# Kernel tuning notes

Hardware: AMD Instinct MI355X
Metric: run time of the kernel (lower is better)

The kernel has to match this reference:

```python
import jax, jax.numpy as jnp
import numpy as np

N = 100000   # nodes
E = 1600000  # edges
F_IN = 32    # num_features
H = 16       # hidden_size (hardcoded as conv2 input in source)
C = 10       # num_classes
K = 2        # kernel_size (dim=1)


def setup_inputs() -> dict:
    key = jax.random.key(0)
    ks = jax.random.split(key, 9)
    x = jax.random.normal(ks[0], (N, F_IN), dtype=jnp.float32)
    edge_index = jax.random.randint(ks[1], (2, E), 0, N, dtype=jnp.int64)
    edge_attr = jax.random.uniform(ks[2], (E, 1), dtype=jnp.float32)
    s1 = 1.0 / np.sqrt(F_IN)
    s2 = 1.0 / np.sqrt(H)
    W1 = jax.random.normal(ks[3], (K, F_IN, H), dtype=jnp.float32) * s1
    root1 = jax.random.normal(ks[4], (F_IN, H), dtype=jnp.float32) * s1
    b1 = jnp.zeros((H,), dtype=jnp.float32)
    W2 = jax.random.normal(ks[5], (K, H, C), dtype=jnp.float32) * s2
    root2 = jax.random.normal(ks[6], (H, C), dtype=jnp.float32) * s2
    b2 = jnp.zeros((C,), dtype=jnp.float32)
    return {"x": x, "edge_index": edge_index, "edge_attr": edge_attr,
            "W1": W1, "root1": root1, "b1": b1,
            "W2": W2, "root2": root2, "b2": b2}


def spline_conv(x, edge_index, edge_attr, W, root, bias, num_nodes):
    # Open B-spline, degree 1: hat-function basis over K knots.
    k = W.shape[0]
    src, dst = edge_index[0], edge_index[1]
    v = edge_attr[:, 0] * (k - 1)                                   # [E]
    grid = jnp.arange(k, dtype=v.dtype)
    basis = jnp.maximum(0.0, 1.0 - jnp.abs(v[:, None] - grid[None, :]))  # [E,K]
    xe = x[src]                                                      # [E,in] gather
    msg = jnp.einsum('ei,kio,ek->eo', xe, W, basis)                  # per-edge message
    agg = jax.ops.segment_sum(msg, dst, num_segments=num_nodes)      # scatter-add
    deg = jax.ops.segment_sum(jnp.ones((msg.shape[0],), x.dtype), dst,
                              num_segments=num_nodes)
    agg = agg / jnp.maximum(deg, 1.0)[:, None]                       # mean aggregation
    return agg + x @ root + bias


def reference(x, edge_index, edge_attr, W1, root1, b1, W2, root2, b2):
    # Inference mode: F.dropout(training=False) is identity.
    h = jax.nn.elu(spline_conv(x, edge_index, edge_attr, W1, root1, b1, N))
    out = spline_conv(h, edge_index, edge_attr, W2, root2, b2, N)
    return jax.nn.log_softmax(out, axis=1)
```

## Files before the change

kernel.cpp:

```cpp
#include <hip/hip_runtime.h>
#include <math.h>

#define N_NODES 100000
#define E_EDGES 1600000
#define F_IN 32
#define HID 16
#define NC 10
#define SRC_BITS 17
#define SRC_MASK ((1u << SRC_BITS) - 1u)
#define VQ_SCALE 32767.0f
#define CBITS 8
#define BUCKET_N 256
#define NCB ((N_NODES + BUCKET_N - 1) / BUCKET_N)
#define BLK_E 4096
#define NBLK ((E_EDGES + BLK_E - 1) / BLK_E)
#define L1_BLOCKS ((N_NODES + 511) / 512)
#define CAP 6144

__device__ __forceinline__ unsigned int bf16pair(float lo, float hi) {
    unsigned int ulo = __float_as_uint(lo), uhi = __float_as_uint(hi);
    ulo += 0x7fffu + ((ulo >> 16) & 1u);
    uhi += 0x7fffu + ((uhi >> 16) & 1u);
    return (ulo >> 16) | (uhi & 0xffff0000u);
}

__device__ __forceinline__ float lerp_pair(unsigned int pair, float v) {
    float a = __uint_as_float(pair << 16);
    float b = __uint_as_float(pair & 0xffff0000u);
    return fmaf(v, b - a, a);
}

__global__ __launch_bounds__(512) void fused_l1bucket(
    const float* __restrict__ x, const float* __restrict__ W1,
    const float* __restrict__ root1, const float* __restrict__ b1,
    const int* __restrict__ ei, const float* __restrict__ ea,
    unsigned int* __restrict__ y, float* __restrict__ r1,
    int* __restrict__ gcur, int2* __restrict__ ebuf)
{
    if (blockIdx.x >= L1_BLOCKS) {
        __shared__ int h[NCB], base[NCB], cur[NCB];
        int t = threadIdx.x;
        int b = blockIdx.x - L1_BLOCKS;
        for (int i = t; i < NCB; i += 512) { h[i] = 0; cur[i] = 0; }
        __syncthreads();

        const int* dstp = ei + E_EDGES;
        int e0 = b * BLK_E + t * 8;
        int4 dA, dB, sA, sB;
        float4 aA, aB;
        bool fullA = (e0 + 3 < E_EDGES), fullB = (e0 + 7 < E_EDGES);
        if (fullA) {
            dA = *(const int4*)(dstp + e0);
            sA = *(const int4*)(ei + e0);
            aA = *(const float4*)(ea + e0);
            atomicAdd(&h[dA.x >> CBITS], 1);
            atomicAdd(&h[dA.y >> CBITS], 1);
            atomicAdd(&h[dA.z >> CBITS], 1);
            atomicAdd(&h[dA.w >> CBITS], 1);
        }
        if (fullB) {
            dB = *(const int4*)(dstp + e0 + 4);
            sB = *(const int4*)(ei + e0 + 4);
            aB = *(const float4*)(ea + e0 + 4);
            atomicAdd(&h[dB.x >> CBITS], 1);
            atomicAdd(&h[dB.y >> CBITS], 1);
            atomicAdd(&h[dB.z >> CBITS], 1);
            atomicAdd(&h[dB.w >> CBITS], 1);
        }
        if (!fullA || !fullB) {
            int lo = fullA ? e0 + 4 : e0;
            for (int e = lo; e < E_EDGES && e < e0 + 8; e++)
                atomicAdd(&h[dstp[e] >> CBITS], 1);
        }
        __syncthreads();

        for (int s = t; s < NCB; s += 512)
            if (h[s] > 0) base[s] = atomicAdd(&gcur[s], h[s]);
        __syncthreads();

        if (fullA) {
            {
                int s = dA.x >> CBITS;
                int idx = base[s] + atomicAdd(&cur[s], 1);
                unsigned int vq = (unsigned int)(aA.x * VQ_SCALE + 0.5f);
                if (idx < CAP)
                    ebuf[(size_t)s * CAP + idx] = make_int2(dA.x & (BUCKET_N - 1),
                        (int)((vq << SRC_BITS) | (unsigned int)sA.x));
            }
            {
                int s = dA.y >> CBITS;
                int idx = base[s] + atomicAdd(&cur[s], 1);
                unsigned int vq = (unsigned int)(aA.y * VQ_SCALE + 0.5f);
                if (idx < CAP)
                    ebuf[(size_t)s * CAP + idx] = make_int2(dA.y & (BUCKET_N - 1),
                        (int)((vq << SRC_BITS) | (unsigned int)sA.y));
            }
            {
                int s = dA.z >> CBITS;
                int idx = base[s] + atomicAdd(&cur[s], 1);
                unsigned int vq = (unsigned int)(aA.z * VQ_SCALE + 0.5f);
                if (idx < CAP)
                    ebuf[(size_t)s * CAP + idx] = make_int2(dA.z & (BUCKET_N - 1),
                        (int)((vq << SRC_BITS) | (unsigned int)sA.z));
            }
            {
                int s = dA.w >> CBITS;
                int idx = base[s] + atomicAdd(&cur[s], 1);
                unsigned int vq = (unsigned int)(aA.w * VQ_SCALE + 0.5f);
                if (idx < CAP)
                    ebuf[(size_t)s * CAP + idx] = make_int2(dA.w & (BUCKET_N - 1),
                        (int)((vq << SRC_BITS) | (unsigned int)sA.w));
            }
        }
        if (fullB) {
            {
                int s = dB.x >> CBITS;
                int idx = base[s] + atomicAdd(&cur[s], 1);
                unsigned int vq = (unsigned int)(aB.x * VQ_SCALE + 0.5f);
                if (idx < CAP)
                    ebuf[(size_t)s * CAP + idx] = make_int2(dB.x & (BUCKET_N - 1),
                        (int)((vq << SRC_BITS) | (unsigned int)sB.x));
            }
            {
                int s = dB.y >> CBITS;
                int idx = base[s] + atomicAdd(&cur[s], 1);
                unsigned int vq = (unsigned int)(aB.y * VQ_SCALE + 0.5f);
                if (idx < CAP)
                    ebuf[(size_t)s * CAP + idx] = make_int2(dB.y & (BUCKET_N - 1),
                        (int)((vq << SRC_BITS) | (unsigned int)sB.y));
            }
            {
                int s = dB.z >> CBITS;
                int idx = base[s] + atomicAdd(&cur[s], 1);
                unsigned int vq = (unsigned int)(aB.z * VQ_SCALE + 0.5f);
                if (idx < CAP)
                    ebuf[(size_t)s * CAP + idx] = make_int2(dB.z & (BUCKET_N - 1),
                        (int)((vq << SRC_BITS) | (unsigned int)sB.z));
            }
            {
                int s = dB.w >> CBITS;
                int idx = base[s] + atomicAdd(&cur[s], 1);
                unsigned int vq = (unsigned int)(aB.w * VQ_SCALE + 0.5f);
                if (idx < CAP)
                    ebuf[(size_t)s * CAP + idx] = make_int2(dB.w & (BUCKET_N - 1),
                        (int)((vq << SRC_BITS) | (unsigned int)sB.w));
            }
        }
        if (!fullA || !fullB) {
            int lo = fullA ? e0 + 4 : e0;
            for (int e = lo; e < E_EDGES && e < e0 + 8; e++) {
                int dst = dstp[e];
                int s = dst >> CBITS;
                int idx = base[s] + atomicAdd(&cur[s], 1);
                unsigned int vq = (unsigned int)(ea[e] * VQ_SCALE + 0.5f);
                if (idx < CAP)
                    ebuf[(size_t)s * CAP + idx] = make_int2(dst & (BUCKET_N - 1),
                        (int)((vq << SRC_BITS) | (unsigned int)ei[e]));
            }
        }
        return;
    }
    __shared__ float sW0[F_IN * HID], sW1[F_IN * HID], sR[F_IN * HID], sB[HID];
    for (int i = threadIdx.x; i < F_IN * HID; i += 512) {
        sW0[i] = W1[i];
        sW1[i] = W1[F_IN * HID + i];
        sR[i]  = root1[i];
    }
    if (threadIdx.x < HID) sB[threadIdx.x] = b1[threadIdx.x];
    __syncthreads();

    int n = blockIdx.x * 512 + threadIdx.x;
    if (n >= N_NODES) return;

    float xr[F_IN];
    const float4* xp = (const float4*)(x + (size_t)n * F_IN);
    #pragma unroll
    for (int i = 0; i < F_IN / 4; i++) {
        float4 t4 = xp[i];
        xr[i*4+0] = t4.x; xr[i*4+1] = t4.y; xr[i*4+2] = t4.z; xr[i*4+3] = t4.w;
    }

    float a0[HID], a1[HID], ar[HID];
    #pragma unroll
    for (int o = 0; o < HID; o++) { a0[o] = 0.f; a1[o] = 0.f; ar[o] = sB[o]; }
    for (int i = 0; i < F_IN; i++) {
        float xi = xr[i];
        #pragma unroll
        for (int o = 0; o < HID; o++) {
            a0[o] += xi * sW0[i * HID + o];
            a1[o] += xi * sW1[i * HID + o];
            ar[o] += xi * sR[i * HID + o];
        }
    }
    unsigned int* py = y + (size_t)n * 16;
    float* pr = r1 + (size_t)n * HID;
    #pragma unroll
    for (int o = 0; o < HID; o++) {
        py[o] = bf16pair(a0[o], a1[o]);
        pr[o] = ar[o];
    }
}

__global__ __launch_bounds__(1024) void k_bsort(
    const int2* __restrict__ ebuf, const int* __restrict__ gcur,
    unsigned int* __restrict__ es, int* __restrict__ start)
{
    __shared__ int hist[BUCKET_N];
    __shared__ int cursor[BUCKET_N];
    __shared__ int pre[NCB];
    __shared__ int wsum[16], woff[16];
    __shared__ int wsum2[4], woff2[4];
    int t = threadIdx.x;
    int b = blockIdx.x;
    int w = t >> 6, l = t & 63;

    int v = (t < NCB) ? min(gcur[t], CAP) : 0;
    int incl = v;
    #pragma unroll
    for (int off = 1; off < 64; off <<= 1) {
        int u = __shfl_up(incl, off, 64);
        if (l >= off) incl += u;
    }
    if (l == 63) wsum[w] = incl;
    if (t < BUCKET_N) { hist[t] = 0; cursor[t] = 0; }
    __syncthreads();
    if (t == 0) {
        int a = 0;
        #pragma unroll
        for (int i = 0; i < 16; i++) { woff[i] = a; a += wsum[i]; }
    }
    __syncthreads();
    if (t < NCB) pre[t] = woff[w] + incl - v;
    __syncthreads();

    int fill = min(gcur[b], CAP);
    int obase = pre[b];
    const int2* win = ebuf + (size_t)b * CAP;

    for (int j = t; j < fill; j += 1024)
        atomicAdd(&hist[win[j].x], 1);
    __syncthreads();

    int c = (t < BUCKET_N) ? hist[t] : 0;
    int incl2 = c;
    #pragma unroll
    for (int off = 1; off < 64; off <<= 1) {
        int u = __shfl_up(incl2, off, 64);
        if (l >= off) incl2 += u;
    }
    if (w < 4 && l == 63) wsum2[w] = incl2;
    __syncthreads();
    if (t == 0) {
        int acc = 0;
        #pragma unroll
        for (int i = 0; i < 4; i++) { woff2[i] = acc; acc += wsum2[i]; }
    }
    __syncthreads();
    if (t < BUCKET_N) {
        int excl = woff2[w] + incl2 - c;
        hist[t] = excl;
        int node = (b << CBITS) + t;
        if (node < N_NODES) start[node] = obase + excl;
    }
    if (b == 0 && t == 0) start[N_NODES] = E_EDGES;
    __syncthreads();

    for (int j = t; j < fill; j += 1024) {
        int2 p = win[j];
        int off = atomicAdd(&cursor[p.x], 1);
        es[obase + hist[p.x] + off] = (unsigned int)p.y;
    }
}

__global__ __launch_bounds__(256) void k_agg1(
    const unsigned int* __restrict__ es, const int* __restrict__ start,
    const unsigned int* __restrict__ y, const float* __restrict__ r1,
    const float* __restrict__ W2, const float* __restrict__ root2,
    const float* __restrict__ b2,
    unsigned int* __restrict__ z, float* __restrict__ r2)
{
    __shared__ float sW0[HID * NC], sW1[HID * NC], sRt[HID * NC], sB2[NC];
    int t = threadIdx.x;
    if (t < HID * NC) { sW0[t] = W2[t]; sW1[t] = W2[HID * NC + t]; sRt[t] = root2[t]; }
    if (t >= HID * NC && t < HID * NC + NC) sB2[t - HID * NC] = b2[t - HID * NC];
    __syncthreads();

    int idx = blockIdx.x * 256 + t;
    int n = idx >> 2, l = idx & 3;
    if (n >= N_NODES) return;
    int j0 = start[n], j1 = start[n + 1];
    const uint4* yrow = (const uint4*)y;
    float acc[4] = {0.f, 0.f, 0.f, 0.f};
    int j = j0;
    for (; j + 3 < j1; j += 4) {
        unsigned int p0 = es[j], p1 = es[j+1], p2 = es[j+2], p3 = es[j+3];
        uint4 q0 = yrow[(size_t)(p0 & SRC_MASK) * 4 + l];
        uint4 q1 = yrow[(size_t)(p1 & SRC_MASK) * 4 + l];
        uint4 q2 = yrow[(size_t)(p2 & SRC_MASK) * 4 + l];
        uint4 q3 = yrow[(size_t)(p3 & SRC_MASK) * 4 + l];
        float v0 = (float)(p0 >> SRC_BITS) * (1.0f / VQ_SCALE);
        float v1 = (float)(p1 >> SRC_BITS) * (1.0f / VQ_SCALE);
        float v2 = (float)(p2 >> SRC_BITS) * (1.0f / VQ_SCALE);
        float v3 = (float)(p3 >> SRC_BITS) * (1.0f / VQ_SCALE);
        acc[0] += lerp_pair(q0.x, v0); acc[1] += lerp_pair(q0.y, v0);
        acc[2] += lerp_pair(q0.z, v0); acc[3] += lerp_pair(q0.w, v0);
        acc[0] += lerp_pair(q1.x, v1); acc[1] += lerp_pair(q1.y, v1);
        acc[2] += lerp_pair(q1.z, v1); acc[3] += lerp_pair(q1.w, v1);
        acc[0] += lerp_pair(q2.x, v2); acc[1] += lerp_pair(q2.y, v2);
        acc[2] += lerp_pair(q2.z, v2); acc[3] += lerp_pair(q2.w, v2);
        acc[0] += lerp_pair(q3.x, v3); acc[1] += lerp_pair(q3.y, v3);
        acc[2] += lerp_pair(q3.z, v3); acc[3] += lerp_pair(q3.w, v3);
    }
    for (; j < j1; j++) {
        unsigned int p = es[j];
        uint4 q = yrow[(size_t)(p & SRC_MASK) * 4 + l];
        float v = (float)(p >> SRC_BITS) * (1.0f / VQ_SCALE);
        acc[0] += lerp_pair(q.x, v); acc[1] += lerp_pair(q.y, v);
        acc[2] += lerp_pair(q.z, v); acc[3] += lerp_pair(q.w, v);
    }
    float inv = 1.0f / fmaxf((float)(j1 - j0), 1.0f);
    float4 rr = *(const float4*)(r1 + (size_t)n * HID + l * 4);
    float hv[4];
    hv[0] = acc[0] * inv + rr.x;
    hv[1] = acc[1] * inv + rr.y;
    hv[2] = acc[2] * inv + rr.z;
    hv[3] = acc[3] * inv + rr.w;
    #pragma unroll
    for (int e = 0; e < 4; e++) hv[e] = hv[e] > 0.0f ? hv[e] : expm1f(hv[e]);

    int cbase = l * 4;
    float a0[4] = {0.f, 0.f, 0.f, 0.f}, a1[4] = {0.f, 0.f, 0.f, 0.f}, ar[4];
    #pragma unroll
    for (int e = 0; e < 4; e++) { int c = cbase + e; ar[e] = (c < NC) ? sB2[c] : 0.f; }
    #pragma unroll
    for (int s = 0; s < 4; s++) {
        #pragma unroll
        for (int e2 = 0; e2 < 4; e2++) {
            float hi = __shfl(hv[e2], s, 4);
            int i = s * 4 + e2;
            #pragma unroll
            for (int e = 0; e < 4; e++) {
                int c = cbase + e;
                if (c < NC) {
                    a0[e] += hi * sW0[i * NC + c];
                    a1[e] += hi * sW1[i * NC + c];
                    ar[e] += hi * sRt[i * NC + c];
                }
            }
        }
    }
    uint4 zo;
    zo.x = (cbase + 0 < NC) ? bf16pair(a0[0], a1[0]) : 0u;
    zo.y = (cbase + 1 < NC) ? bf16pair(a0[1], a1[1]) : 0u;
    zo.z = (cbase + 2 < NC) ? bf16pair(a0[2], a1[2]) : 0u;
    zo.w = (cbase + 3 < NC) ? bf16pair(a0[3], a1[3]) : 0u;
    ((uint4*)z)[(size_t)n * 4 + l] = zo;
    #pragma unroll
    for (int e = 0; e < 4; e++) {
        int c = cbase + e;
        if (c < NC) r2[(size_t)n * NC + c] = ar[e];
    }
}

__global__ __launch_bounds__(256) void k_agg2(
    const unsigned int* __restrict__ es, const int* __restrict__ start,
    const unsigned int* __restrict__ z,
    const float* __restrict__ r2, float* __restrict__ out)
{
    int idx = blockIdx.x * 256 + threadIdx.x;
    int n = idx >> 2, l = idx & 3;
    if (n >= N_NODES) return;
    int j0 = start[n], j1 = start[n + 1];
    const uint4* zrow = (const uint4*)z;
    float acc[4] = {0.f, 0.f, 0.f, 0.f};
    int j = j0;
    for (; j + 3 < j1; j += 4) {
        unsigned int p0 = es[j], p1 = es[j+1], p2 = es[j+2], p3 = es[j+3];
        uint4 q0 = zrow[(size_t)(p0 & SRC_MASK) * 4 + l];
        uint4 q1 = zrow[(size_t)(p1 & SRC_MASK) * 4 + l];
        uint4 q2 = zrow[(size_t)(p2 & SRC_MASK) * 4 + l];
        uint4 q3 = zrow[(size_t)(p3 & SRC_MASK) * 4 + l];
        float v0 = (float)(p0 >> SRC_BITS) * (1.0f / VQ_SCALE);
        float v1 = (float)(p1 >> SRC_BITS) * (1.0f / VQ_SCALE);
        float v2 = (float)(p2 >> SRC_BITS) * (1.0f / VQ_SCALE);
        float v3 = (float)(p3 >> SRC_BITS) * (1.0f / VQ_SCALE);
        acc[0] += lerp_pair(q0.x, v0); acc[1] += lerp_pair(q0.y, v0);
        acc[2] += lerp_pair(q0.z, v0); acc[3] += lerp_pair(q0.w, v0);
        acc[0] += lerp_pair(q1.x, v1); acc[1] += lerp_pair(q1.y, v1);
        acc[2] += lerp_pair(q1.z, v1); acc[3] += lerp_pair(q1.w, v1);
        acc[0] += lerp_pair(q2.x, v2); acc[1] += lerp_pair(q2.y, v2);
        acc[2] += lerp_pair(q2.z, v2); acc[3] += lerp_pair(q2.w, v2);
        acc[0] += lerp_pair(q3.x, v3); acc[1] += lerp_pair(q3.y, v3);
        acc[2] += lerp_pair(q3.z, v3); acc[3] += lerp_pair(q3.w, v3);
    }
    for (; j < j1; j++) {
        unsigned int p = es[j];
        uint4 q = zrow[(size_t)(p & SRC_MASK) * 4 + l];
        float v = (float)(p >> SRC_BITS) * (1.0f / VQ_SCALE);
        acc[0] += lerp_pair(q.x, v); acc[1] += lerp_pair(q.y, v);
        acc[2] += lerp_pair(q.z, v); acc[3] += lerp_pair(q.w, v);
    }
    float inv = 1.0f / fmaxf((float)(j1 - j0), 1.0f);
    int cbase = l * 4;
    float val[4];
    #pragma unroll
    for (int e = 0; e < 4; e++) {
        int c = cbase + e;
        val[e] = (c < NC) ? acc[e] * inv + r2[(size_t)n * NC + c] : -INFINITY;
    }
    float mx = fmaxf(fmaxf(val[0], val[1]), fmaxf(val[2], val[3]));
    mx = fmaxf(mx, __shfl_xor(mx, 1, 4));
    mx = fmaxf(mx, __shfl_xor(mx, 2, 4));
    float ssum = 0.f;
    #pragma unroll
    for (int e = 0; e < 4; e++) {
        int c = cbase + e;
        if (c < NC) ssum += expf(val[e] - mx);
    }
    ssum += __shfl_xor(ssum, 1, 4);
    ssum += __shfl_xor(ssum, 2, 4);
    float lse = logf(ssum);
    #pragma unroll
    for (int e = 0; e < 4; e++) {
        int c = cbase + e;
        if (c < NC) out[(size_t)n * NC + c] = val[e] - mx - lse;
    }
}

extern "C" void kernel_launch(void* const* d_in, const int* in_sizes, int n_in,
                              void* d_out, int out_size, void* d_ws, size_t ws_size,
                              hipStream_t stream) {
    const float* x     = (const float*)d_in[0];
    const int*   ei    = (const int*)d_in[1];
    const float* ea    = (const float*)d_in[2];
    const float* W1    = (const float*)d_in[3];
    const float* root1 = (const float*)d_in[4];
    const float* b1    = (const float*)d_in[5];
    const float* W2    = (const float*)d_in[6];
    const float* root2 = (const float*)d_in[7];
    const float* b2    = (const float*)d_in[8];
    float* out = (float*)d_out;

    char* wsb = (char*)d_ws;
    int2*         ebuf   = (int2*)wsb;
    unsigned int* es     = (unsigned int*)(wsb + (size_t)NCB * CAP * 8);
    unsigned int* y      = es + (size_t)E_EDGES;
    float*        r1     = (float*)(y + (size_t)N_NODES * 16);
    unsigned int* z      = (unsigned int*)(r1 + (size_t)N_NODES * HID);
    float*        r2     = (float*)(z + (size_t)N_NODES * 16);
    int*          start  = (int*)(r2 + (size_t)N_NODES * NC);
    int*          gcur   = start + N_NODES + 1;

    int aggGrid = (N_NODES * 4 + 255) / 256;

    hipMemsetAsync(gcur, 0, (size_t)NCB * sizeof(int), stream);
    fused_l1bucket<<<L1_BLOCKS + NBLK, 512, 0, stream>>>(x, W1, root1, b1, ei, ea,
                                                         y, r1, gcur, ebuf);
    k_bsort<<<NCB, 1024, 0, stream>>>(ebuf, gcur, es, start);
    k_agg1 <<<aggGrid, 256, 0, stream>>>(es, start, y, r1, W2, root2, b2, z, r2);
    k_agg2 <<<aggGrid, 256, 0, stream>>>(es, start, z, r2, out);
}
```

Before: 176.1 us.

## Split bucket buffer into byte and word arrays, enlarge edge blocks, unroll gathers

Replaces the int2 bucket buffer with a separate byte array for the local destination and a word array for the packed payload. This cuts bucket-stage write and read traffic from 8 to 5 bytes per edge. Doubles the edges handled per scatter block (16 per thread) to amortize the shared histogram setup and the global atomics. Adds 8-way unrolled gather loops to both aggregation kernels for more memory-level parallelism, at the cost of higher register pressure.

```diff
diff --git a/kernel.cpp b/kernel.cpp
--- a/kernel.cpp
+++ b/kernel.cpp
@@ -12,7 +12,7 @@
 #define CBITS 8
 #define BUCKET_N 256
 #define NCB ((N_NODES + BUCKET_N - 1) / BUCKET_N)
-#define BLK_E 4096
+#define BLK_E 8192
 #define NBLK ((E_EDGES + BLK_E - 1) / BLK_E)
 #define L1_BLOCKS ((N_NODES + 511) / 512)
 #define CAP 6144
@@ -35,7 +35,8 @@
     const float* __restrict__ root1, const float* __restrict__ b1,
     const int* __restrict__ ei, const float* __restrict__ ea,
     unsigned int* __restrict__ y, float* __restrict__ r1,
-    int* __restrict__ gcur, int2* __restrict__ ebuf)
+    int* __restrict__ gcur,
+    unsigned char* __restrict__ ebufd, unsigned int* __restrict__ ebufp)
 {
     if (blockIdx.x >= L1_BLOCKS) {
         __shared__ int h[NCB], base[NCB], cur[NCB];
@@ -45,32 +46,26 @@
         __syncthreads();
 
         const int* dstp = ei + E_EDGES;
-        int e0 = b * BLK_E + t * 8;
-        int4 dA, dB, sA, sB;
-        float4 aA, aB;
-        bool fullA = (e0 + 3 < E_EDGES), fullB = (e0 + 7 < E_EDGES);
-        if (fullA) {
-            dA = *(const int4*)(dstp + e0);
-            sA = *(const int4*)(ei + e0);
-            aA = *(const float4*)(ea + e0);
-            atomicAdd(&h[dA.x >> CBITS], 1);
-            atomicAdd(&h[dA.y >> CBITS], 1);
-            atomicAdd(&h[dA.z >> CBITS], 1);
-            atomicAdd(&h[dA.w >> CBITS], 1);
-        }
-        if (fullB) {
-            dB = *(const int4*)(dstp + e0 + 4);
-            sB = *(const int4*)(ei + e0 + 4);
-            aB = *(const float4*)(ea + e0 + 4);
-            atomicAdd(&h[dB.x >> CBITS], 1);
-            atomicAdd(&h[dB.y >> CBITS], 1);
-            atomicAdd(&h[dB.z >> CBITS], 1);
-            atomicAdd(&h[dB.w >> CBITS], 1);
-        }
-        if (!fullA || !fullB) {
-            int lo = fullA ? e0 + 4 : e0;
-            for (int e = lo; e < E_EDGES && e < e0 + 8; e++)
-                atomicAdd(&h[dstp[e] >> CBITS], 1);
+        int e0 = b * BLK_E + t * 16;
+        int4 d4[4], s4[4];
+        float4 a4[4];
+        int fullmask = 0;
+        #pragma unroll
+        for (int i = 0; i < 4; i++) {
+            int g = e0 + i * 4;
+            if (g + 3 < E_EDGES) {
+                d4[i] = *(const int4*)(dstp + g);
+                s4[i] = *(const int4*)(ei + g);
+                a4[i] = *(const float4*)(ea + g);
+                fullmask |= (1 << i);
+                atomicAdd(&h[d4[i].x >> CBITS], 1);
+                atomicAdd(&h[d4[i].y >> CBITS], 1);
+                atomicAdd(&h[d4[i].z >> CBITS], 1);
+                atomicAdd(&h[d4[i].w >> CBITS], 1);
+            } else {
+                for (int e = g; e < E_EDGES && e < g + 4; e++)
+                    atomicAdd(&h[dstp[e] >> CBITS], 1);
+            }
         }
         __syncthreads();
 
@@ -78,86 +73,31 @@
             if (h[s] > 0) base[s] = atomicAdd(&gcur[s], h[s]);
         __syncthreads();
 
-        if (fullA) {
-            {
-                int s = dA.x >> CBITS;
-                int idx = base[s] + atomicAdd(&cur[s], 1);
-                unsigned int vq = (unsigned int)(aA.x * VQ_SCALE + 0.5f);
-                if (idx < CAP)
-                    ebuf[(size_t)s * CAP + idx] = make_int2(dA.x & (BUCKET_N - 1),
-                        (int)((vq << SRC_BITS) | (unsigned int)sA.x));
-            }
-            {
-                int s = dA.y >> CBITS;
-                int idx = base[s] + atomicAdd(&cur[s], 1);
-                unsigned int vq = (unsigned int)(aA.y * VQ_SCALE + 0.5f);
-                if (idx < CAP)
-                    ebuf[(size_t)s * CAP + idx] = make_int2(dA.y & (BUCKET_N - 1),
-                        (int)((vq << SRC_BITS) | (unsigned int)sA.y));
-            }
-            {
-                int s = dA.z >> CBITS;
-                int idx = base[s] + atomicAdd(&cur[s], 1);
-                unsigned int vq = (unsigned int)(aA.z * VQ_SCALE + 0.5f);
-                if (idx < CAP)
-                    ebuf[(size_t)s * CAP + idx] = make_int2(dA.z & (BUCKET_N - 1),
-                        (int)((vq << SRC_BITS) | (unsigned int)sA.z));
-            }
-            {
-                int s = dA.w >> CBITS;
-                int idx = base[s] + atomicAdd(&cur[s], 1);
-                unsigned int vq = (unsigned int)(aA.w * VQ_SCALE + 0.5f);
-                if (idx < CAP)
-                    ebuf[(size_t)s * CAP + idx] = make_int2(dA.w & (BUCKET_N - 1),
-                        (int)((vq << SRC_BITS) | (unsigned int)sA.w));
+        #define SCAT(dv, sv, av) do {                                           \
+            int s_ = (dv) >> CBITS;                                             \
+            int idx_ = base[s_] + atomicAdd(&cur[s_], 1);                       \
+            if (idx_ < CAP) {                                                   \
+                size_t o_ = (size_t)s_ * CAP + idx_;                            \
+                ebufd[o_] = (unsigned char)((dv) & (BUCKET_N - 1));             \
+                unsigned int vq_ = (unsigned int)((av) * VQ_SCALE + 0.5f);      \
+                ebufp[o_] = (vq_ << SRC_BITS) | (unsigned int)(sv);             \
+            }                                                                   \
+        } while (0)
+
+        #pragma unroll
+        for (int i = 0; i < 4; i++) {
+            if (fullmask & (1 << i)) {
+                SCAT(d4[i].x, s4[i].x, a4[i].x);
+                SCAT(d4[i].y, s4[i].y, a4[i].y);
+                SCAT(d4[i].z, s4[i].z, a4[i].z);
+                SCAT(d4[i].w, s4[i].w, a4[i].w);
+            } else {
+                int g = e0 + i * 4;
+                for (int e = g; e < E_EDGES && e < g + 4; e++)
+                    SCAT(dstp[e], ei[e], ea[e]);
             }
         }
-        if (fullB) {
-            {
-                int s = dB.x >> CBITS;
-                int idx = base[s] + atomicAdd(&cur[s], 1);
-                unsigned int vq = (unsigned int)(aB.x * VQ_SCALE + 0.5f);
-                if (idx < CAP)
-                    ebuf[(size_t)s * CAP + idx] = make_int2(dB.x & (BUCKET_N - 1),
-                        (int)((vq << SRC_BITS) | (unsigned int)sB.x));
-            }
-            {
-                int s = dB.y >> CBITS;
-                int idx = base[s] + atomicAdd(&cur[s], 1);
-                unsigned int vq = (unsigned int)(aB.y * VQ_SCALE + 0.5f);
-                if (idx < CAP)
-                    ebuf[(size_t)s * CAP + idx] = make_int2(dB.y & (BUCKET_N - 1),
-                        (int)((vq << SRC_BITS) | (unsigned int)sB.y));
-            }
-            {
-                int s = dB.z >> CBITS;
-                int idx = base[s] + atomicAdd(&cur[s], 1);
-                unsigned int vq = (unsigned int)(aB.z * VQ_SCALE + 0.5f);
-                if (idx < CAP)
-                    ebuf[(size_t)s * CAP + idx] = make_int2(dB.z & (BUCKET_N - 1),
-                        (int)((vq << SRC_BITS) | (unsigned int)sB.z));
-            }
-            {
-                int s = dB.w >> CBITS;
-                int idx = base[s] + atomicAdd(&cur[s], 1);
-                unsigned int vq = (unsigned int)(aB.w * VQ_SCALE + 0.5f);
-                if (idx < CAP)
-                    ebuf[(size_t)s * CAP + idx] = make_int2(dB.w & (BUCKET_N - 1),
-                        (int)((vq << SRC_BITS) | (unsigned int)sB.w));
-            }
-        }
-        if (!fullA || !fullB) {
-            int lo = fullA ? e0 + 4 : e0;
-            for (int e = lo; e < E_EDGES && e < e0 + 8; e++) {
-                int dst = dstp[e];
-                int s = dst >> CBITS;
-                int idx = base[s] + atomicAdd(&cur[s], 1);
-                unsigned int vq = (unsigned int)(ea[e] * VQ_SCALE + 0.5f);
-                if (idx < CAP)
-                    ebuf[(size_t)s * CAP + idx] = make_int2(dst & (BUCKET_N - 1),
-                        (int)((vq << SRC_BITS) | (unsigned int)ei[e]));
-            }
-        }
+        #undef SCAT
         return;
     }
     __shared__ float sW0[F_IN * HID], sW1[F_IN * HID], sR[F_IN * HID], sB[HID];
@@ -202,7 +142,8 @@
 }
 
 __global__ __launch_bounds__(1024) void k_bsort(
-    const int2* __restrict__ ebuf, const int* __restrict__ gcur,
+    const unsigned char* __restrict__ ebufd, const unsigned int* __restrict__ ebufp,
+    const int* __restrict__ gcur,
     unsigned int* __restrict__ es, int* __restrict__ start)
 {
     __shared__ int hist[BUCKET_N];
@@ -235,10 +176,11 @@
 
     int fill = min(gcur[b], CAP);
     int obase = pre[b];
-    const int2* win = ebuf + (size_t)b * CAP;
+    const unsigned char* wind = ebufd + (size_t)b * CAP;
+    const unsigned int*  winp = ebufp + (size_t)b * CAP;
 
     for (int j = t; j < fill; j += 1024)
-        atomicAdd(&hist[win[j].x], 1);
+        atomicAdd(&hist[wind[j]], 1);
     __syncthreads();
 
     int c = (t < BUCKET_N) ? hist[t] : 0;
@@ -266,9 +208,9 @@
     __syncthreads();
 
     for (int j = t; j < fill; j += 1024) {
-        int2 p = win[j];
-        int off = atomicAdd(&cursor[p.x], 1);
-        es[obase + hist[p.x] + off] = (unsigned int)p.y;
+        int d = wind[j];
+        int off = atomicAdd(&cursor[d], 1);
+        es[obase + hist[d] + off] = winp[j];
     }
 }
 
@@ -292,6 +234,42 @@
     const uint4* yrow = (const uint4*)y;
     float acc[4] = {0.f, 0.f, 0.f, 0.f};
     int j = j0;
+    for (; j + 7 < j1; j += 8) {
+        unsigned int p0 = es[j],   p1 = es[j+1], p2 = es[j+2], p3 = es[j+3];
+        unsigned int p4 = es[j+4], p5 = es[j+5], p6 = es[j+6], p7 = es[j+7];
+        uint4 q0 = yrow[(size_t)(p0 & SRC_MASK) * 4 + l];
+        uint4 q1 = yrow[(size_t)(p1 & SRC_MASK) * 4 + l];
+        uint4 q2 = yrow[(size_t)(p2 & SRC_MASK) * 4 + l];
+        uint4 q3 = yrow[(size_t)(p3 & SRC_MASK) * 4 + l];
+        uint4 q4 = yrow[(size_t)(p4 & SRC_MASK) * 4 + l];
+        uint4 q5 = yrow[(size_t)(p5 & SRC_MASK) * 4 + l];
+        uint4 q6 = yrow[(size_t)(p6 & SRC_MASK) * 4 + l];
+        uint4 q7 = yrow[(size_t)(p7 & SRC_MASK) * 4 + l];
+        float v0 = (float)(p0 >> SRC_BITS) * (1.0f / VQ_SCALE);
+        float v1 = (float)(p1 >> SRC_BITS) * (1.0f / VQ_SCALE);
+        float v2 = (float)(p2 >> SRC_BITS) * (1.0f / VQ_SCALE);
+        float v3 = (float)(p3 >> SRC_BITS) * (1.0f / VQ_SCALE);
+        float v4 = (float)(p4 >> SRC_BITS) * (1.0f / VQ_SCALE);
+        float v5 = (float)(p5 >> SRC_BITS) * (1.0f / VQ_SCALE);
+        float v6 = (float)(p6 >> SRC_BITS) * (1.0f / VQ_SCALE);
+        float v7 = (float)(p7 >> SRC_BITS) * (1.0f / VQ_SCALE);
+        acc[0] += lerp_pair(q0.x, v0); acc[1] += lerp_pair(q0.y, v0);
+        acc[2] += lerp_pair(q0.z, v0); acc[3] += lerp_pair(q0.w, v0);
+        acc[0] += lerp_pair(q1.x, v1); acc[1] += lerp_pair(q1.y, v1);
+        acc[2] += lerp_pair(q1.z, v1); acc[3] += lerp_pair(q1.w, v1);
+        acc[0] += lerp_pair(q2.x, v2); acc[1] += lerp_pair(q2.y, v2);
+        acc[2] += lerp_pair(q2.z, v2); acc[3] += lerp_pair(q2.w, v2);
+        acc[0] += lerp_pair(q3.x, v3); acc[1] += lerp_pair(q3.y, v3);
+        acc[2] += lerp_pair(q3.z, v3); acc[3] += lerp_pair(q3.w, v3);
+        acc[0] += lerp_pair(q4.x, v4); acc[1] += lerp_pair(q4.y, v4);
+        acc[2] += lerp_pair(q4.z, v4); acc[3] += lerp_pair(q4.w, v4);
+        acc[0] += lerp_pair(q5.x, v5); acc[1] += lerp_pair(q5.y, v5);
+        acc[2] += lerp_pair(q5.z, v5); acc[3] += lerp_pair(q5.w, v5);
+        acc[0] += lerp_pair(q6.x, v6); acc[1] += lerp_pair(q6.y, v6);
+        acc[2] += lerp_pair(q6.z, v6); acc[3] += lerp_pair(q6.w, v6);
+        acc[0] += lerp_pair(q7.x, v7); acc[1] += lerp_pair(q7.y, v7);
+        acc[2] += lerp_pair(q7.z, v7); acc[3] += lerp_pair(q7.w, v7);
+    }
     for (; j + 3 < j1; j += 4) {
         unsigned int p0 = es[j], p1 = es[j+1], p2 = es[j+2], p3 = es[j+3];
         uint4 q0 = yrow[(size_t)(p0 & SRC_MASK) * 4 + l];
@@ -374,6 +352,42 @@
     const uint4* zrow = (const uint4*)z;
     float acc[4] = {0.f, 0.f, 0.f, 0.f};
     int j = j0;
+    for (; j + 7 < j1; j += 8) {
+        unsigned int p0 = es[j],   p1 = es[j+1], p2 = es[j+2], p3 = es[j+3];
+        unsigned int p4 = es[j+4], p5 = es[j+5], p6 = es[j+6], p7 = es[j+7];
+        uint4 q0 = zrow[(size_t)(p0 & SRC_MASK) * 4 + l];
+        uint4 q1 = zrow[(size_t)(p1 & SRC_MASK) * 4 + l];
+        uint4 q2 = zrow[(size_t)(p2 & SRC_MASK) * 4 + l];
+        uint4 q3 = zrow[(size_t)(p3 & SRC_MASK) * 4 + l];
+        uint4 q4 = zrow[(size_t)(p4 & SRC_MASK) * 4 + l];
+        uint4 q5 = zrow[(size_t)(p5 & SRC_MASK) * 4 + l];
+        uint4 q6 = zrow[(size_t)(p6 & SRC_MASK) * 4 + l];
+        uint4 q7 = zrow[(size_t)(p7 & SRC_MASK) * 4 + l];
+        float v0 = (float)(p0 >> SRC_BITS) * (1.0f / VQ_SCALE);
+        float v1 = (float)(p1 >> SRC_BITS) * (1.0f / VQ_SCALE);
+        float v2 = (float)(p2 >> SRC_BITS) * (1.0f / VQ_SCALE);
+        float v3 = (float)(p3 >> SRC_BITS) * (1.0f / VQ_SCALE);
+        float v4 = (float)(p4 >> SRC_BITS) * (1.0f / VQ_SCALE);
+        float v5 = (float)(p5 >> SRC_BITS) * (1.0f / VQ_SCALE);
+        float v6 = (float)(p6 >> SRC_BITS) * (1.0f / VQ_SCALE);
+        float v7 = (float)(p7 >> SRC_BITS) * (1.0f / VQ_SCALE);
+        acc[0] += lerp_pair(q0.x, v0); acc[1] += lerp_pair(q0.y, v0);
+        acc[2] += lerp_pair(q0.z, v0); acc[3] += lerp_pair(q0.w, v0);
+        acc[0] += lerp_pair(q1.x, v1); acc[1] += lerp_pair(q1.y, v1);
+        acc[2] += lerp_pair(q1.z, v1); acc[3] += lerp_pair(q1.w, v1);
+        acc[0] += lerp_pair(q2.x, v2); acc[1] += lerp_pair(q2.y, v2);
+        acc[2] += lerp_pair(q2.z, v2); acc[3] += lerp_pair(q2.w, v2);
+        acc[0] += lerp_pair(q3.x, v3); acc[1] += lerp_pair(q3.y, v3);
+        acc[2] += lerp_pair(q3.z, v3); acc[3] += lerp_pair(q3.w, v3);
+        acc[0] += lerp_pair(q4.x, v4); acc[1] += lerp_pair(q4.y, v4);
+        acc[2] += lerp_pair(q4.z, v4); acc[3] += lerp_pair(q4.w, v4);
+        acc[0] += lerp_pair(q5.x, v5); acc[1] += lerp_pair(q5.y, v5);
+        acc[2] += lerp_pair(q5.z, v5); acc[3] += lerp_pair(q5.w, v5);
+        acc[0] += lerp_pair(q6.x, v6); acc[1] += lerp_pair(q6.y, v6);
+        acc[2] += lerp_pair(q6.z, v6); acc[3] += lerp_pair(q6.w, v6);
+        acc[0] += lerp_pair(q7.x, v7); acc[1] += lerp_pair(q7.y, v7);
+        acc[2] += lerp_pair(q7.z, v7); acc[3] += lerp_pair(q7.w, v7);
+    }
     for (; j + 3 < j1; j += 4) {
         unsigned int p0 = es[j], p1 = es[j+1], p2 = es[j+2], p3 = es[j+3];
         uint4 q0 = zrow[(size_t)(p0 & SRC_MASK) * 4 + l];
@@ -442,21 +456,22 @@
     float* out = (float*)d_out;
 
     char* wsb = (char*)d_ws;
-    int2*         ebuf   = (int2*)wsb;
-    unsigned int* es     = (unsigned int*)(wsb + (size_t)NCB * CAP * 8);
+    unsigned int* ebufp  = (unsigned int*)wsb;
+    unsigned int* es     = ebufp + (size_t)NCB * CAP;
     unsigned int* y      = es + (size_t)E_EDGES;
     float*        r1     = (float*)(y + (size_t)N_NODES * 16);
     unsigned int* z      = (unsigned int*)(r1 + (size_t)N_NODES * HID);
     float*        r2     = (float*)(z + (size_t)N_NODES * 16);
     int*          start  = (int*)(r2 + (size_t)N_NODES * NC);
     int*          gcur   = start + N_NODES + 1;
+    unsigned char* ebufd = (unsigned char*)(gcur + NCB);
 
     int aggGrid = (N_NODES * 4 + 255) / 256;
 
     hipMemsetAsync(gcur, 0, (size_t)NCB * sizeof(int), stream);
     fused_l1bucket<<<L1_BLOCKS + NBLK, 512, 0, stream>>>(x, W1, root1, b1, ei, ea,
-                                                         y, r1, gcur, ebuf);
-    k_bsort<<<NCB, 1024, 0, stream>>>(ebuf, gcur, es, start);
+                                                         y, r1, gcur, ebufd, ebufp);
+    k_bsort<<<NCB, 1024, 0, stream>>>(ebufd, ebufp, gcur, es, start);
     k_agg1 <<<aggGrid, 256, 0, stream>>>(es, start, y, r1, W2, root2, b2, z, r2);
     k_agg2 <<<aggGrid, 256, 0, stream>>>(es, start, z, r2, out);
 }
```

After: 188.0 us. +6.8%, slower.
